# Kernel tuning notes

Measured on AMD Instinct MI355X. Metric: run time of the kernel, lower is better.

## Reference

```python
import jax, jax.numpy as jnp
import numpy as np
from math import factorial

# ---- static config mirroring Cace.__init__ ----
MAX_L = 3            # max angular degree
N_RBF = 8            # Bessel radial basis size
RB = 8               # n_radial_basis (radial embedding dim after transform)
K = 3                # n_atom_basis -> edge channels C = K*K
NZ = 4               # len(zs)
CUTOFF = 5.5
N_NODES = 2000
N_EDGES = 50000
T_MP = 1             # num_message_passing
MP_NORM = 1.0 / np.sqrt(25.0)   # 1/sqrt(avg_num_neighbors)
C = K * K

def _lxlylz(max_l):
    out = []
    for l in range(max_l + 1):
        for lx in range(l, -1, -1):
            for ly in range(l - lx, -1, -1):
                out.append((lx, ly, l - lx - ly))
    return out

L_LIST = _lxlylz(MAX_L)                 # 20 Cartesian monomials for max_l=3
NL = len(L_LIST)
LX = np.array([t[0] for t in L_LIST]); LY = np.array([t[1] for t in L_LIST]); LZ = np.array([t[2] for t in L_LIST])
DEGS = LX + LY + LZ                     # degree l of each monomial
MULTI = np.array([factorial(int(d)) / (factorial(int(a)) * factorial(int(b)) * factorial(int(c)))
                  for a, b, c, d in zip(LX, LY, LZ, DEGS)], dtype=np.float32)
SEL = np.zeros((NL, MAX_L + 1), np.float32)
SEL[np.arange(NL), DEGS] = 1.0          # monomial -> degree one-hot (for per-l sums)
NB = 1 + (MAX_L + 1)                    # symmetrizer feats: nu=1 (l=0) + nu=2 per l

def bessel(r):  # [E] -> [E, N_RBF]
    n = jnp.arange(1, N_RBF + 1, dtype=r.dtype)
    return jnp.sqrt(2.0 / CUTOFF) * jnp.sin(n[None, :] * jnp.pi * r[:, None] / CUTOFF) / r[:, None]

def poly_cutoff(r):  # MACE-style polynomial cutoff, p=6
    p = 6.0
    u = r / CUTOFF
    f = 1.0 - (p + 1.0) * (p + 2.0) / 2.0 * u**6 + p * (p + 2.0) * u**7 - p * (p + 1.0) / 2.0 * u**8
    return f * (u < 1.0)

def axis_pows(x):  # [E] -> [E, MAX_L+1] = x^0..x^MAX_L (safe grads, handles negatives)
    pows = [jnp.ones_like(x)]
    for _ in range(MAX_L):
        pows.append(pows[-1] * x)
    return jnp.stack(pows, axis=1)

def angular(u):  # unit vectors [E,3] -> Cartesian monomials [E, NL]
    return axis_pows(u[:, 0])[:, LX] * axis_pows(u[:, 1])[:, LY] * axis_pows(u[:, 2])[:, LZ]

def radial_transform(x, W):  # x [N,R,L,C], W [MAX_L+1,R,Rb] shared per degree l
    return jnp.einsum('nrlc,lrb->nblc', x, W[DEGS])

def symmetrize(A):  # A [N,Rb,NL,C] -> B [N,Rb,NB,C]
    b1 = A[:, :, :1, :]  # nu=1: the (0,0,0) monomial (index 0)
    w = (A * A) * jnp.asarray(MULTI)[None, None, :, None]
    b2 = jnp.einsum('nrlc,lm->nrmc', w, jnp.asarray(SEL))  # nu=2 invariant per degree l
    return jnp.concatenate([b1, b2], axis=2)


def setup_inputs() -> dict:
    key = jax.random.key(0)
    ks = jax.random.split(key, 9)
    positions = jax.random.uniform(ks[0], (N_NODES, 3), dtype=jnp.float32) * 12.0
    species = jax.random.randint(ks[1], (N_NODES,), 0, NZ)
    send = jax.random.randint(ks[2], (N_EDGES,), 0, N_NODES)
    off = jax.random.randint(ks[3], (N_EDGES,), 1, N_NODES)
    recv = (send + off) % N_NODES  # no self-edges -> strictly positive edge lengths
    edge_index = jnp.stack([send, recv])
    shifts = jnp.zeros((N_EDGES, 3), jnp.float32)
    W_embed = jax.random.normal(ks[4], (NZ, K), jnp.float32)
    W_radial = jax.random.normal(ks[5], (MAX_L + 1, N_RBF, RB), jnp.float32) / np.sqrt(N_RBF)
    W_mem = jax.random.normal(ks[6], (MAX_L + 1, RB, RB), jnp.float32) / np.sqrt(RB)
    W_ar = jax.random.normal(ks[7], (N_RBF, RB), jnp.float32) / np.sqrt(N_RBF)
    W_chi = jax.random.normal(ks[8], (RB, NB), jnp.float32) * 0.1
    return {"positions": positions, "shifts": shifts, "W_embed": W_embed, "W_radial": W_radial,
            "W_mem": W_mem, "W_ar": W_ar, "W_chi": W_chi, "species": species, "edge_index": edge_index}


def reference(positions, shifts, W_embed, W_radial, W_mem, W_ar, W_chi, species, edge_index):
    n_nodes = positions.shape[0]
    send, recv = edge_index[0], edge_index[1]
    # edge geometry
    vec = positions[recv] - positions[send] + shifts
    lengths = jnp.linalg.norm(vec, axis=-1)
    u = vec / (lengths[:, None] + 1e-9)
    rad = bessel(lengths)          # [E,R]
    fcut = poly_cutoff(lengths)    # [E]
    ang = angular(u)               # [E,NL]
    # edge type encoding: outer product of sender/receiver species embeddings
    emb = W_embed[species]         # [N,K]
    enc = (emb[send][:, :, None] * emb[recv][:, None, :]).reshape(-1, C)  # [E,C]
    # elementwise_multiply_3tensors -> [E,R,NL,C]
    edge_attri = jnp.einsum('er,el,ec->erlc', rad * fcut[:, None], ang, enc)
    A = radial_transform(jax.ops.segment_sum(edge_attri, recv, num_segments=n_nodes), W_radial)  # [N,Rb,NL,C]
    B = symmetrize(A)              # [N,Rb,NB,C]
    feats = [B]
    for _ in range(T_MP):
        mem = jnp.einsum('nrlc,lrb->nblc', A, W_mem[DEGS])        # NodeMemory
        chi = jnp.einsum('nbkc,bk->nc', B, W_chi)                  # MessageBchi node scalar
        msg_bchi = edge_attri * chi[send][:, None, None, :]
        A_bchi = radial_transform(jax.ops.segment_sum(msg_bchi, recv, num_segments=n_nodes), W_radial)
        fr = (rad @ W_ar) * fcut[:, None]                          # MessageAr radial filter [E,Rb]
        msg_ar = A[send] * fr[:, :, None, None]
        A_ar = jax.ops.segment_sum(msg_ar, recv, num_segments=n_nodes)
        A = (A_ar + A_bchi) * MP_NORM + mem
        B = symmetrize(A)
        feats.append(B)
    return jnp.stack(feats, axis=-1)   # [N,Rb,NB,C,T_MP+1]
```

## Files before the change

### kernel.cpp

```cpp
#include <hip/hip_runtime.h>
#include <hip/hip_bf16.h>


#define CUTF 5.5f
#define MPNORM 0.2f

__constant__ int   d_DEGS[20]  = {0,1,1,1,2,2,2,2,2,2,3,3,3,3,3,3,3,3,3,3};
__constant__ float d_MULTI[20] = {1,1,1,1,1,2,2,1,2,1,1,3,3,3,6,3,1,3,3,1};

__global__ void k_count(const int* __restrict__ eidx, int* __restrict__ counts,
                        int* __restrict__ erank, int E) {
  int e = blockIdx.x * blockDim.x + threadIdx.x;
  if (e < E) erank[e] = atomicAdd(&counts[eidx[E + e]], 1);
}

__global__ void k_scan(const int* __restrict__ counts, int* __restrict__ offs, int N) {
  __shared__ int part[256];
  int t = threadIdx.x;
  int local[8]; int sum = 0;
  #pragma unroll
  for (int i = 0; i < 8; i++) {
    int idx = t*8 + i;
    int v = (idx < N) ? counts[idx] : 0;
    local[i] = sum; sum += v;
  }
  part[t] = sum; __syncthreads();
  for (int d = 1; d < 256; d <<= 1) {
    int add = (t >= d) ? part[t-d] : 0;
    __syncthreads();
    part[t] += add;
    __syncthreads();
  }
  int excl = part[t] - sum;
  #pragma unroll
  for (int i = 0; i < 8; i++) {
    int idx = t*8 + i;
    if (idx < N) offs[idx] = excl + local[i];
  }
  if (t == 255) offs[N] = part[255];
}

__global__ __launch_bounds__(64) void k_edge(
                       const float* __restrict__ pos,
                       const float* __restrict__ shifts,
                       const float* __restrict__ Wemb,
                       const float* __restrict__ War,
                       const int* __restrict__ species,
                       const int* __restrict__ eidx,
                       const int* __restrict__ offs,
                       const int* __restrict__ erank,
                       float* __restrict__ edata,
                       int* __restrict__ esend,
                       int E) {
  __shared__ float war_s[64];
  int t = threadIdx.x;
  war_s[t] = War[t];
  __syncthreads();
  int e = blockIdx.x * 64 + t;
  if (e >= E) return;
  int s  = eidx[e];
  int rI = eidx[E + e];
  int rk = erank[e];
  float vx = pos[rI*3+0] - pos[s*3+0] + shifts[e*3+0];
  float vy = pos[rI*3+1] - pos[s*3+1] + shifts[e*3+1];
  float vz = pos[rI*3+2] - pos[s*3+2] + shifts[e*3+2];
  float len = sqrtf(vx*vx + vy*vy + vz*vz);
  float inv = 1.0f / (len + 1e-9f);
  float ux = vx*inv, uy = vy*inv, uz = vz*inv;
  float uu = len * (1.0f/CUTF);
  float u2 = uu*uu, u6 = u2*u2*u2;
  float fcut = (uu < 1.0f) ? (1.0f - 28.0f*u6 + 48.0f*u6*uu - 21.0f*u6*u2) : 0.0f;
  float x = 3.14159265358979f * uu;
  float sn = sinf(x), c2 = 2.0f*cosf(x), snm1 = 0.0f;
  float pref = sqrtf(2.0f/CUTF) / (len + 1e-20f);
  float rad[8];
  float v[48];
  #pragma unroll
  for (int k = 0; k < 8; k++) {
    rad[k] = pref * sn;
    v[k]   = rad[k] * fcut;
    float nxt = c2*sn - snm1; snm1 = sn; sn = nxt;
  }
  #pragma unroll
  for (int b = 0; b < 8; b++) {
    float a = 0.0f;
    #pragma unroll
    for (int k = 0; k < 8; k++) a += rad[k] * war_s[k*8+b];
    v[8+b] = a * fcut;
  }
  float px2 = ux*ux, py2 = uy*uy, pz2 = uz*uz;
  v[16] = 1.0f; v[17] = ux;     v[18] = uy;     v[19] = uz;
  v[20] = px2;  v[21] = ux*uy;  v[22] = ux*uz;  v[23] = py2;
  v[24] = uy*uz;v[25] = pz2;
  v[26] = px2*ux; v[27] = px2*uy; v[28] = px2*uz; v[29] = ux*py2;
  v[30] = ux*uy*uz; v[31] = ux*pz2; v[32] = py2*uy; v[33] = py2*uz;
  v[34] = uy*pz2; v[35] = pz2*uz;
  int zs = species[s], zr = species[rI];
  float es0 = Wemb[zs*3+0], es1 = Wemb[zs*3+1], es2 = Wemb[zs*3+2];
  float er0 = Wemb[zr*3+0], er1 = Wemb[zr*3+1], er2 = Wemb[zr*3+2];
  v[36] = es0*er0; v[37] = es0*er1; v[38] = es0*er2;
  v[39] = es1*er0; v[40] = es1*er1; v[41] = es1*er2;
  v[42] = es2*er0; v[43] = es2*er1; v[44] = es2*er2;
  v[45] = 0.0f; v[46] = 0.0f; v[47] = 0.0f;
  int dst = offs[rI] + rk;
  float4* eb4 = reinterpret_cast<float4*>(edata + (size_t)dst * 48);
  #pragma unroll
  for (int w = 0; w < 12; w++)
    eb4[w] = make_float4(v[4*w], v[4*w+1], v[4*w+2], v[4*w+3]);
  esend[dst] = s;
}

__global__ __launch_bounds__(192) void k_nodeA(
    const float* __restrict__ edata, const int* __restrict__ offs,
    const float* __restrict__ Wrad, const float* __restrict__ Wchi,
    float* __restrict__ A, uint2* __restrict__ Abf2lo, uint2* __restrict__ Abf2hi,
    float* __restrict__ chi, float* __restrict__ B0, int N) {
  __shared__ float wr_s[288];
  __shared__ float wchi_s[40];
  __shared__ float Bsh[360];
  int t = threadIdx.x, n = blockIdx.x;
  for (int i = t; i < 256; i += 192) { int d = i >> 6, rm = i & 63; wr_s[d*72+rm] = Wrad[i]; }
  for (int i = t; i < 40;  i += 192) wchi_s[i] = Wchi[i];
  for (int i = t; i < 360; i += 192) Bsh[i] = 0.0f;
  int l = t / 9, c = t - l*9;
  bool act = t < 180;
  int ll = act ? l : 0, cc = act ? c : 0;
  float acc[8];
  #pragma unroll
  for (int r = 0; r < 8; r++) acc[r] = 0.0f;
  int start = offs[n], end = offs[n+1];
  #pragma unroll 4
  for (int j = start; j < end; j++) {
    const float* row = edata + (size_t)j * 48;
    float p = row[16+ll] * row[36+cc];
    #pragma unroll
    for (int r = 0; r < 8; r++) acc[r] += row[r] * p;
  }
  __syncthreads();
  int deg = act ? d_DEGS[ll] : 0;
  const float* wp = &wr_s[deg*72];
  float Ab[8];
  #pragma unroll
  for (int b = 0; b < 8; b++) {
    float a = 0.0f;
    #pragma unroll
    for (int r = 0; r < 8; r++) a += acc[r] * wp[r*8+b];
    Ab[b] = a;
  }
  if (act) {
    #pragma unroll
    for (int b = 0; b < 8; b++) A[(size_t)n*1440 + t*8 + b] = Ab[b];
    unsigned int pk[4];
    #pragma unroll
    for (int bp = 0; bp < 4; bp++) {
      __hip_bfloat16 blo = __float2bfloat16(Ab[2*bp]);
      __hip_bfloat16 bhi = __float2bfloat16(Ab[2*bp+1]);
      pk[bp] = (unsigned int)(*reinterpret_cast<unsigned short*>(&blo))
             | ((unsigned int)(*reinterpret_cast<unsigned short*>(&bhi)) << 16);
    }
    uint2 qlo; qlo.x = pk[0]; qlo.y = pk[1];
    uint2 qhi; qhi.x = pk[2]; qhi.y = pk[3];
    Abf2lo[(size_t)n*180 + t] = qlo;
    Abf2hi[(size_t)n*180 + t] = qhi;
    if (l == 0) {
      #pragma unroll
      for (int b = 0; b < 8; b++) Bsh[b*45 + c] = Ab[b];
    }
    float mlt = d_MULTI[ll]; int kk = 1 + deg;
    #pragma unroll
    for (int b = 0; b < 8; b++) atomicAdd(&Bsh[b*45 + kk*9 + c], mlt*Ab[b]*Ab[b]);
  }
  __syncthreads();
  if (t < 9) {
    float s = 0.0f;
    for (int b = 0; b < 8; b++)
      #pragma unroll
      for (int kq = 0; kq < 5; kq++) s += Bsh[b*45 + kq*9 + t] * wchi_s[b*5 + kq];
    chi[n*9 + t] = s;
  }
  for (int i = t; i < 360; i += 192)
    B0[(size_t)n*360 + i] = Bsh[i];
}

__global__ __launch_bounds__(192) void k_node2(
    const float* __restrict__ edata, const int* __restrict__ esend,
    const int* __restrict__ offs,
    const float* __restrict__ Wrad, const float* __restrict__ Wmem,
    const float* __restrict__ A,
    const uint2* __restrict__ Abf2lo, const uint2* __restrict__ Abf2hi,
    const float* __restrict__ chi, const float* __restrict__ B0,
    float* __restrict__ out, int N) {
  __shared__ float wr_s[288], wm_s[288];
  __shared__ float Bsh[360];
  int t = threadIdx.x, n = blockIdx.x;
  for (int i = t; i < 256; i += 192) {
    int d = i >> 6, rm = i & 63;
    wr_s[d*72+rm] = Wrad[i];
    wm_s[d*72+rm] = Wmem[i];
  }
  for (int i = t; i < 360; i += 192) Bsh[i] = 0.0f;
  int l = t / 9, c = t - l*9;
  bool act = t < 180;
  int ll = act ? l : 0, cc = act ? c : 0;
  int tt = act ? t : 0;
  float Sacc[8], ARacc[8];
  #pragma unroll
  for (int r = 0; r < 8; r++) { Sacc[r] = 0.0f; ARacc[r] = 0.0f; }
  int start = offs[n], end = offs[n+1];
  #pragma unroll 4
  for (int j = start; j < end; j++) {
    const float* row = edata + (size_t)j * 48;
    int snd = esend[j];
    float ch = chi[snd*9 + cc];
    const uint2 ql = Abf2lo[(size_t)snd*180 + tt];
    float pch = row[16+ll] * row[36+cc] * ch;
    #pragma unroll
    for (int r = 0; r < 8; r++) Sacc[r] += row[r] * pch;
    float a0 = __uint_as_float(ql.x << 16), a1 = __uint_as_float(ql.x & 0xffff0000u);
    float a2 = __uint_as_float(ql.y << 16), a3 = __uint_as_float(ql.y & 0xffff0000u);
    ARacc[0] += a0*row[8];  ARacc[1] += a1*row[9];
    ARacc[2] += a2*row[10]; ARacc[3] += a3*row[11];
  }
  #pragma unroll 4
  for (int j = start; j < end; j++) {
    const float* row = edata + (size_t)j * 48;
    int snd = esend[j];
    const uint2 qh = Abf2hi[(size_t)snd*180 + tt];
    float a4 = __uint_as_float(qh.x << 16), a5 = __uint_as_float(qh.x & 0xffff0000u);
    float a6 = __uint_as_float(qh.y << 16), a7 = __uint_as_float(qh.y & 0xffff0000u);
    ARacc[4] += a4*row[12]; ARacc[5] += a5*row[13];
    ARacc[6] += a6*row[14]; ARacc[7] += a7*row[15];
  }
  __syncthreads();
  if (act) {
    int deg = d_DEGS[ll];
    const float* wrp = &wr_s[deg*72];
    const float* wmp = &wm_s[deg*72];
    const float* aop = A + (size_t)n*1440 + t*8;
    float aown[8];
    #pragma unroll
    for (int r = 0; r < 8; r++) aown[r] = aop[r];
    float newA[8];
    #pragma unroll
    for (int b = 0; b < 8; b++) {
      float mem = 0.0f, ab = 0.0f;
      #pragma unroll
      for (int r = 0; r < 8; r++) { mem += aown[r]*wmp[r*8+b]; ab += Sacc[r]*wrp[r*8+b]; }
      newA[b] = (ARacc[b] + ab)*MPNORM + mem;
    }
    if (l == 0) {
      #pragma unroll
      for (int b = 0; b < 8; b++) Bsh[b*45 + c] = newA[b];
    }
    float mlt = d_MULTI[ll]; int kk = 1 + deg;
    #pragma unroll
    for (int b = 0; b < 8; b++) atomicAdd(&Bsh[b*45 + kk*9 + c], mlt*newA[b]*newA[b]);
  }
  __syncthreads();
  float2* out2 = reinterpret_cast<float2*>(out);
  for (int i = t; i < 360; i += 192) {
    float2 pk; pk.x = B0[(size_t)n*360 + i]; pk.y = Bsh[i];
    out2[(size_t)n*360 + i] = pk;
  }
}

extern "C" void kernel_launch(void* const* d_in, const int* in_sizes, int n_in,
                              void* d_out, int out_size, void* d_ws, size_t ws_size,
                              hipStream_t stream) {
  const float* pos    = (const float*)d_in[0];
  const float* shifts = (const float*)d_in[1];
  const float* Wemb   = (const float*)d_in[2];
  const float* Wrad   = (const float*)d_in[3];
  const float* Wmem   = (const float*)d_in[4];
  const float* War    = (const float*)d_in[5];
  const float* Wchi   = (const float*)d_in[6];
  const int* species = (const int*)d_in[7];
  const int* eidx    = (const int*)d_in[8];
  float* out = (float*)d_out;
  int N = in_sizes[7];
  int E = in_sizes[8] / 2;

  char* base = (char*)d_ws;
  size_t off = 0;
  float* edata = (float*)(base + off); off += (size_t)E*48*4;
  float* A     = (float*)(base + off); off += (size_t)N*1440*4;
  uint2* Abf2lo = (uint2*)(base + off); off += (size_t)N*180*8;
  uint2* Abf2hi = (uint2*)(base + off); off += (size_t)N*180*8;
  float* chi   = (float*)(base + off); off += (size_t)N*9*4;
  float* B0    = (float*)(base + off); off += (size_t)N*360*4;
  int* counts  = (int*)(base + off);   off += (size_t)N*4;
  int* offs    = (int*)(base + off);   off += (((size_t)(N+1)*4) + 15) & ~(size_t)15;
  int* esend   = (int*)(base + off);   off += (size_t)E*4;
  int* erank   = (int*)(base + off);   off += (((size_t)E*4) + 15) & ~(size_t)15;

  hipMemsetAsync(counts, 0, (size_t)N*4, stream);
  k_count<<<(E + 255) / 256, 256, 0, stream>>>(eidx, counts, erank, E);
  k_scan<<<1, 256, 0, stream>>>(counts, offs, N);
  k_edge<<<(E + 63) / 64, 64, 0, stream>>>(pos, shifts, Wemb, War, species, eidx,
                                           offs, erank, edata, esend, E);
  k_nodeA<<<N, 192, 0, stream>>>(edata, offs, Wrad, Wchi, A, Abf2lo, Abf2hi, chi, B0, N);
  k_node2<<<N, 192, 0, stream>>>(edata, esend, offs, Wrad, Wmem, A, Abf2lo, Abf2hi,
                                 chi, B0, out, N);
}
```

Measured before the change: 158.3 us.

## Schedule node blocks by descending degree and merge bf16 A gathers into one pass

The scan kernel now builds a degree histogram and a counting sort, so nodeA and node2 blocks are launched in descending in-degree order to even out load across the tail of the grid. The two split bf16 copies of A (lo/hi halves) become a single 16-byte-per-thread array, and node2 does its sender gathers in one edge loop instead of two. This removes a second pass over edata, esend and the gathered rows. In exchange it adds serial work to the single-block scan kernel and uses an extra level of indirection for the node index.

Measured after the change: 155.7 us. No clear change (-1.6%).

```diff
diff --git a/kernel.cpp b/kernel.cpp
--- a/kernel.cpp
+++ b/kernel.cpp
@@ -14,15 +14,21 @@
   if (e < E) erank[e] = atomicAdd(&counts[eidx[E + e]], 1);
 }
 
-__global__ void k_scan(const int* __restrict__ counts, int* __restrict__ offs, int N) {
+__global__ void k_scan(const int* __restrict__ counts, int* __restrict__ offs,
+                       int* __restrict__ nodeorder, int N) {
   __shared__ int part[256];
+  __shared__ int hist[256];
+  __shared__ int hoff[256];
   int t = threadIdx.x;
-  int local[8]; int sum = 0;
+  hist[t] = 0;
+  __syncthreads();
+  int local[8]; int deg8[8]; int sum = 0;
   #pragma unroll
   for (int i = 0; i < 8; i++) {
     int idx = t*8 + i;
     int v = (idx < N) ? counts[idx] : 0;
-    local[i] = sum; sum += v;
+    local[i] = sum; sum += v; deg8[i] = v;
+    if (idx < N) atomicAdd(&hist[v > 255 ? 255 : v], 1);
   }
   part[t] = sum; __syncthreads();
   for (int d = 1; d < 256; d <<= 1) {
@@ -38,6 +44,27 @@
     if (idx < N) offs[idx] = excl + local[i];
   }
   if (t == 255) offs[N] = part[255];
+  __syncthreads();
+  int h = hist[t];
+  part[t] = hist[255 - t];
+  __syncthreads();
+  for (int d = 1; d < 256; d <<= 1) {
+    int add = (t >= d) ? part[t-d] : 0;
+    __syncthreads();
+    part[t] += add;
+    __syncthreads();
+  }
+  hoff[t] = part[255 - t] - h;
+  __syncthreads();
+  #pragma unroll
+  for (int i = 0; i < 8; i++) {
+    int idx = t*8 + i;
+    if (idx < N) {
+      int dg = deg8[i] > 255 ? 255 : deg8[i];
+      int pos = atomicAdd(&hoff[dg], 1);
+      nodeorder[pos] = idx;
+    }
+  }
 }
 
 __global__ __launch_bounds__(64) void k_edge(
@@ -112,13 +139,15 @@
 
 __global__ __launch_bounds__(192) void k_nodeA(
     const float* __restrict__ edata, const int* __restrict__ offs,
+    const int* __restrict__ nodeorder,
     const float* __restrict__ Wrad, const float* __restrict__ Wchi,
-    float* __restrict__ A, uint2* __restrict__ Abf2lo, uint2* __restrict__ Abf2hi,
+    float* __restrict__ A, uint4* __restrict__ Abf2,
     float* __restrict__ chi, float* __restrict__ B0, int N) {
   __shared__ float wr_s[288];
   __shared__ float wchi_s[40];
   __shared__ float Bsh[360];
-  int t = threadIdx.x, n = blockIdx.x;
+  int t = threadIdx.x;
+  int n = nodeorder[blockIdx.x];
   for (int i = t; i < 256; i += 192) { int d = i >> 6, rm = i & 63; wr_s[d*72+rm] = Wrad[i]; }
   for (int i = t; i < 40;  i += 192) wchi_s[i] = Wchi[i];
   for (int i = t; i < 360; i += 192) Bsh[i] = 0.0f;
@@ -158,10 +187,8 @@
       pk[bp] = (unsigned int)(*reinterpret_cast<unsigned short*>(&blo))
              | ((unsigned int)(*reinterpret_cast<unsigned short*>(&bhi)) << 16);
     }
-    uint2 qlo; qlo.x = pk[0]; qlo.y = pk[1];
-    uint2 qhi; qhi.x = pk[2]; qhi.y = pk[3];
-    Abf2lo[(size_t)n*180 + t] = qlo;
-    Abf2hi[(size_t)n*180 + t] = qhi;
+    uint4 qv; qv.x = pk[0]; qv.y = pk[1]; qv.z = pk[2]; qv.w = pk[3];
+    Abf2[(size_t)n*180 + t] = qv;
     if (l == 0) {
       #pragma unroll
       for (int b = 0; b < 8; b++) Bsh[b*45 + c] = Ab[b];
@@ -184,15 +211,15 @@
 
 __global__ __launch_bounds__(192) void k_node2(
     const float* __restrict__ edata, const int* __restrict__ esend,
-    const int* __restrict__ offs,
+    const int* __restrict__ offs, const int* __restrict__ nodeorder,
     const float* __restrict__ Wrad, const float* __restrict__ Wmem,
-    const float* __restrict__ A,
-    const uint2* __restrict__ Abf2lo, const uint2* __restrict__ Abf2hi,
+    const float* __restrict__ A, const uint4* __restrict__ Abf2,
     const float* __restrict__ chi, const float* __restrict__ B0,
     float* __restrict__ out, int N) {
   __shared__ float wr_s[288], wm_s[288];
   __shared__ float Bsh[360];
-  int t = threadIdx.x, n = blockIdx.x;
+  int t = threadIdx.x;
+  int n = nodeorder[blockIdx.x];
   for (int i = t; i < 256; i += 192) {
     int d = i >> 6, rm = i & 63;
     wr_s[d*72+rm] = Wrad[i];
@@ -212,22 +239,16 @@
     const float* row = edata + (size_t)j * 48;
     int snd = esend[j];
     float ch = chi[snd*9 + cc];
-    const uint2 ql = Abf2lo[(size_t)snd*180 + tt];
     float pch = row[16+ll] * row[36+cc] * ch;
     #pragma unroll
     for (int r = 0; r < 8; r++) Sacc[r] += row[r] * pch;
-    float a0 = __uint_as_float(ql.x << 16), a1 = __uint_as_float(ql.x & 0xffff0000u);
-    float a2 = __uint_as_float(ql.y << 16), a3 = __uint_as_float(ql.y & 0xffff0000u);
+    const uint4 qv = Abf2[(size_t)snd*180 + tt];
+    float a0 = __uint_as_float(qv.x << 16), a1 = __uint_as_float(qv.x & 0xffff0000u);
+    float a2 = __uint_as_float(qv.y << 16), a3 = __uint_as_float(qv.y & 0xffff0000u);
+    float a4 = __uint_as_float(qv.z << 16), a5 = __uint_as_float(qv.z & 0xffff0000u);
+    float a6 = __uint_as_float(qv.w << 16), a7 = __uint_as_float(qv.w & 0xffff0000u);
     ARacc[0] += a0*row[8];  ARacc[1] += a1*row[9];
     ARacc[2] += a2*row[10]; ARacc[3] += a3*row[11];
-  }
-  #pragma unroll 4
-  for (int j = start; j < end; j++) {
-    const float* row = edata + (size_t)j * 48;
-    int snd = esend[j];
-    const uint2 qh = Abf2hi[(size_t)snd*180 + tt];
-    float a4 = __uint_as_float(qh.x << 16), a5 = __uint_as_float(qh.x & 0xffff0000u);
-    float a6 = __uint_as_float(qh.y << 16), a7 = __uint_as_float(qh.y & 0xffff0000u);
     ARacc[4] += a4*row[12]; ARacc[5] += a5*row[13];
     ARacc[6] += a6*row[14]; ARacc[7] += a7*row[15];
   }
@@ -284,21 +305,21 @@
   size_t off = 0;
   float* edata = (float*)(base + off); off += (size_t)E*48*4;
   float* A     = (float*)(base + off); off += (size_t)N*1440*4;
-  uint2* Abf2lo = (uint2*)(base + off); off += (size_t)N*180*8;
-  uint2* Abf2hi = (uint2*)(base + off); off += (size_t)N*180*8;
+  uint4* Abf2  = (uint4*)(base + off); off += (size_t)N*180*16;
   float* chi   = (float*)(base + off); off += (size_t)N*9*4;
   float* B0    = (float*)(base + off); off += (size_t)N*360*4;
   int* counts  = (int*)(base + off);   off += (size_t)N*4;
   int* offs    = (int*)(base + off);   off += (((size_t)(N+1)*4) + 15) & ~(size_t)15;
   int* esend   = (int*)(base + off);   off += (size_t)E*4;
   int* erank   = (int*)(base + off);   off += (((size_t)E*4) + 15) & ~(size_t)15;
+  int* nodeorder = (int*)(base + off); off += (((size_t)N*4) + 15) & ~(size_t)15;
 
   hipMemsetAsync(counts, 0, (size_t)N*4, stream);
   k_count<<<(E + 255) / 256, 256, 0, stream>>>(eidx, counts, erank, E);
-  k_scan<<<1, 256, 0, stream>>>(counts, offs, N);
+  k_scan<<<1, 256, 0, stream>>>(counts, offs, nodeorder, N);
   k_edge<<<(E + 63) / 64, 64, 0, stream>>>(pos, shifts, Wemb, War, species, eidx,
                                            offs, erank, edata, esend, E);
-  k_nodeA<<<N, 192, 0, stream>>>(edata, offs, Wrad, Wchi, A, Abf2lo, Abf2hi, chi, B0, N);
-  k_node2<<<N, 192, 0, stream>>>(edata, esend, offs, Wrad, Wmem, A, Abf2lo, Abf2hi,
+  k_nodeA<<<N, 192, 0, stream>>>(edata, offs, nodeorder, Wrad, Wchi, A, Abf2, chi, B0, N);
+  k_node2<<<N, 192, 0, stream>>>(edata, esend, offs, nodeorder, Wrad, Wmem, A, Abf2,
                                  chi, B0, out, N);
 }
```
